# Kernel optimization log

Hardware: AMD Instinct MI355X
Metric: run time of the kernel (lower is better)

## Reference

```python
import jax, jax.numpy as jnp
import numpy as np

D_K = 1024
NHEADS = 16
HEAD_DIM = D_K // NHEADS  # 64
STD = float(np.sqrt(HEAD_DIM))  # matches math.sqrt(d_k // nheads)


def setup_inputs() -> dict:
    key = jax.random.key(0)
    ks = jax.random.split(key, 9)
    B, S = 2, 2048
    scale = 1.0 / np.sqrt(D_K)
    x = jax.random.normal(ks[0], (B, S, D_K), dtype=jnp.float32)
    Wq = jax.random.normal(ks[1], (D_K, D_K), dtype=jnp.float32) * scale
    bq = jnp.zeros((D_K,), dtype=jnp.float32)
    Wk = jax.random.normal(ks[2], (D_K, D_K), dtype=jnp.float32) * scale
    bk = jnp.zeros((D_K,), dtype=jnp.float32)
    Wv = jax.random.normal(ks[3], (D_K, D_K), dtype=jnp.float32) * scale
    bv = jnp.zeros((D_K,), dtype=jnp.float32)
    Wo = jax.random.normal(ks[4], (D_K, D_K), dtype=jnp.float32) * scale
    bo = jnp.zeros((D_K,), dtype=jnp.float32)
    return {"x": x, "Wq": Wq, "bq": bq, "Wk": Wk, "bk": bk,
            "Wv": Wv, "bv": bv, "Wo": Wo, "bo": bo}


def _heads(x, W, b):
    # Linear then split heads: (B,S,D) -> (B,H,S,hd)
    B, S, _ = x.shape
    out = x @ W.T + b
    return out.reshape(B, S, NHEADS, HEAD_DIM).transpose(0, 2, 1, 3)


def reference(x, Wq, bq, Wk, bk, Wv, bv, Wo, bo):
    B, S, _ = x.shape
    q = _heads(x, Wq, bq)  # (B,H,S,hd)
    k = _heads(x, Wk, bk)
    v = _heads(x, Wv, bv)
    scores = jnp.einsum('bhqd,bhkd->bhqk', q, k) / STD  # (B,H,S,S)
    causal = jnp.tril(jnp.ones((S, S), dtype=bool))  # mask_factory default
    scores = jnp.where(causal[None, None, :, :], scores, -jnp.inf)
    attn = jax.nn.softmax(scores, axis=-1)
    ctx = jnp.einsum('bhqk,bhkd->bhqd', attn, v)  # (B,H,S,hd)
    ctx = ctx.transpose(0, 2, 1, 3).reshape(B, S, D_K)
    return ctx @ Wo.T + bo
```

## Files before the change

### kernel.cpp

```cpp
#include <hip/hip_runtime.h>
#include <stdint.h>

typedef unsigned short u16;
typedef __bf16 bf16x8 __attribute__((ext_vector_type(8)));
typedef __bf16 bf16x4v __attribute__((ext_vector_type(4)));
typedef float f32x4 __attribute__((ext_vector_type(4)));

typedef __attribute__((address_space(3))) uint32_t lds_u32;
typedef __attribute__((address_space(1))) uint32_t glb_u32;

__device__ __forceinline__ f32x4 mfma16(bf16x8 a, bf16x8 b, f32x4 c) {
    return __builtin_amdgcn_mfma_f32_16x16x32_bf16(a, b, c, 0, 0, 0);
}

__device__ __forceinline__ ushort4 pk4(float a, float b, float c, float d) {
    bf16x4v v;
    v[0] = (__bf16)a; v[1] = (__bf16)b; v[2] = (__bf16)c; v[3] = (__bf16)d;
    union { bf16x4v v; ushort4 u; } cv; cv.v = v; return cv.u;
}

__device__ __forceinline__ float fexp2(float x) {
    return __builtin_amdgcn_exp2f(x);
}

__device__ __forceinline__ void async16(const u16* g, u16* l) {
    __builtin_amdgcn_global_load_lds((glb_u32*)(uintptr_t)(const void*)g,
                                     (lds_u32*)l, 16, 0, 0);
}

__global__ __launch_bounds__(256) void cast_all(
    const float* __restrict__ x,
    const float* __restrict__ w0, const float* __restrict__ w1,
    const float* __restrict__ w2, const float* __restrict__ w3,
    u16* __restrict__ xo, u16* __restrict__ o0, u16* __restrict__ o1,
    u16* __restrict__ o2, u16* __restrict__ o3)
{
    const int s = blockIdx.y;
    const int i = (blockIdx.x * 256 + threadIdx.x) * 4;
    if (s == 0) {
#pragma unroll
        for (int c = 0; c < 4; ++c) {
            const int j = i + c * (1 << 20);
            float4 v = *(const float4*)(x + j);
            *(ushort4*)(xo + j) = pk4(v.x, v.y, v.z, v.w);
        }
    } else {
        const float* in = s == 1 ? w0 : (s == 2 ? w1 : (s == 3 ? w2 : w3));
        u16* out       = s == 1 ? o0 : (s == 2 ? o1 : (s == 3 ? o2 : o3));
        float4 v = *(const float4*)(in + i);
        *(ushort4*)(out + i) = pk4(v.x, v.y, v.z, v.w);
    }
}

__global__ __launch_bounds__(256) void gemm_qkv(
    const u16* __restrict__ A,
    const u16* __restrict__ W0, const u16* __restrict__ W1, const u16* __restrict__ W2,
    const float* __restrict__ B0, const float* __restrict__ B1, const float* __restrict__ B2,
    u16* __restrict__ O0, u16* __restrict__ O1,
    u16* __restrict__ VT,
    int M, int N, int K)
{
    const int x = blockIdx.x & 7;
    const int L = blockIdx.x >> 3;
    const int tm = (8 * (x >> 1) + (L & 7)) << 7;
    const int tnsel = 12 * (x & 1) + (L >> 3);
    const int sel = tnsel >> 3;
    const int tn  = (tnsel & 7) << 7;

    const u16* W      = sel == 0 ? W0 : (sel == 1 ? W1 : W2);
    const float* bias = sel == 0 ? B0 : (sel == 1 ? B1 : B2);
    u16* O            = sel == 0 ? O0 : O1;

    __shared__ __attribute__((aligned(16))) u16 As[2][128 * 64];
    __shared__ __attribute__((aligned(16))) u16 Bs[2][128 * 64];
    u16 (*Tb)[136] = (u16 (*)[136])As;

    const int tid  = threadIdx.x;
    const int lane = tid & 63;
    const int w    = tid >> 6;
    const int l15  = lane & 15;
    const int quad = lane >> 4;

    const int wm = (w >> 1) << 6;
    const int wn = (w & 1) << 6;

    f32x4 acc[4][4];
#pragma unroll
    for (int i = 0; i < 4; ++i)
#pragma unroll
        for (int j = 0; j < 4; ++j) acc[i][j] = f32x4{0.f, 0.f, 0.f, 0.f};

    const int lr  = lane >> 3;
    const int lcc = lane & 7;
    const int scc = lcc ^ lr;
    const u16* Ag = A + (size_t)(tm + 32 * w + lr) * K + scc * 8;
    const u16* Wg = W + (size_t)(tn + 32 * w + lr) * K + scc * 8;
    u16* Al = &As[0][(32 * w + lr) * 64 + lcc * 8];
    u16* Bl = &Bs[0][(32 * w + lr) * 64 + lcc * 8];

#define QKV_STAGE(bi, k0)                                                      \
    do {                                                                       \
        _Pragma("unroll")                                                      \
        for (int m = 0; m < 4; ++m) {                                          \
            async16(Ag + (k0) + (size_t)m * 8 * K, Al + (bi) * 8192 + m * 512);\
            async16(Wg + (k0) + (size_t)m * 8 * K, Bl + (bi) * 8192 + m * 512);\
        }                                                                      \
    } while (0)

    const int nt = K >> 6;
    QKV_STAGE(0, 0);
    for (int t = 0; t < nt; ++t) {
        const int cur = t & 1;
        asm volatile("s_waitcnt vmcnt(0)" ::: "memory");
        __syncthreads();
        if (t + 1 < nt) QKV_STAGE(cur ^ 1, (t + 1) * 64);
        const u16* Ab = As[cur];
        const u16* Bb = Bs[cur];
#pragma unroll
        for (int kk = 0; kk < 2; ++kk) {
            bf16x8 a[4], b[4];
#pragma unroll
            for (int i = 0; i < 4; ++i) {
                const int r  = wm + 16 * i + l15;
                const int sl = (kk * 4 + quad) ^ (r & 7);
                a[i] = *(const bf16x8*)&Ab[r * 64 + sl * 8];
            }
#pragma unroll
            for (int j = 0; j < 4; ++j) {
                const int r  = wn + 16 * j + l15;
                const int sl = (kk * 4 + quad) ^ (r & 7);
                b[j] = *(const bf16x8*)&Bb[r * 64 + sl * 8];
            }
#pragma unroll
            for (int i = 0; i < 4; ++i)
#pragma unroll
                for (int j = 0; j < 4; ++j)
                    acc[i][j] = mfma16(a[i], b[j], acc[i][j]);
        }
    }
#undef QKV_STAGE

    if (sel == 2) {
        const int bb = tm >> 11;
        const int s0 = tm & 2047;
        const size_t vtb = ((size_t)bb << 10) + tn;
        for (int c32 = 0; c32 < 128; c32 += 32) {
            __syncthreads();
            if ((c32 >> 6) == (wn >> 6)) {
                const int j0 = (c32 >> 4) & 2;
#pragma unroll
                for (int jj = 0; jj < 2; ++jj) {
                    const int j  = j0 + jj;
                    const int cc = jj * 16 + l15;
                    const float bj = bias[tn + wn + 16 * j + l15];
#pragma unroll
                    for (int i = 0; i < 4; ++i) {
                        const int rr = wm + 16 * i + quad * 4;
                        *(ushort4*)&Tb[cc][rr] =
                            pk4(acc[i][j][0] + bj, acc[i][j][1] + bj,
                                acc[i][j][2] + bj, acc[i][j][3] + bj);
                    }
                }
            }
            __syncthreads();
            {
                const int c  = tid >> 3;
                const int ss = (tid & 7) * 16;
                uint4 v0 = *(const uint4*)&Tb[c][ss];
                uint4 v1 = *(const uint4*)&Tb[c][ss + 8];
                u16* dst = &VT[(vtb + c32 + c) * 2048 + s0 + ss];
                *(uint4*)dst       = v0;
                *(uint4*)(dst + 8) = v1;
            }
        }
    } else {
#pragma unroll
        for (int j = 0; j < 4; ++j) {
            const int col = tn + wn + 16 * j + l15;
            const float bj = bias[col];
#pragma unroll
            for (int i = 0; i < 4; ++i) {
                const int row = tm + wm + 16 * i + quad * 4;
#pragma unroll
                for (int r = 0; r < 4; ++r) {
                    union { float f; unsigned u; } v; v.f = acc[i][j][r] + bj;
                    unsigned rn = v.u + 0x7FFFu + ((v.u >> 16) & 1u);
                    O[(size_t)(row + r) * N + col] = (u16)(rn >> 16);
                }
            }
        }
    }
}

__global__ __launch_bounds__(256) void gemm_out64(
    const u16* __restrict__ A, const u16* __restrict__ W,
    const float* __restrict__ bias, float* __restrict__ O,
    int M, int N, int K)
{
    __shared__ __attribute__((aligned(16))) u16 As[2][128 * 64];
    __shared__ __attribute__((aligned(16))) u16 Bs[2][64 * 64];

    const int x = blockIdx.x & 7;
    const int L = blockIdx.x >> 3;
    const int tm = (8 * (x >> 1) + (L & 7)) << 7;
    const int tn = (8 * (x & 1) + (L >> 3)) << 6;

    const int tid  = threadIdx.x;
    const int lane = tid & 63;
    const int w    = tid >> 6;
    const int l15  = lane & 15;
    const int quad = lane >> 4;

    const int wm = (w >> 1) << 6;
    const int wn = (w & 1) << 5;

    f32x4 acc[4][2];
#pragma unroll
    for (int i = 0; i < 4; ++i)
#pragma unroll
        for (int j = 0; j < 2; ++j) acc[i][j] = f32x4{0.f, 0.f, 0.f, 0.f};

    const int lr  = lane >> 3;
    const int lcc = lane & 7;
    const int scc = lcc ^ lr;
    const u16* Ag = A + (size_t)(tm + 32 * w + lr) * K + scc * 8;
    const u16* Wg = W + (size_t)(tn + 16 * w + lr) * K + scc * 8;
    u16* Al = &As[0][(32 * w + lr) * 64 + lcc * 8];
    u16* Bl = &Bs[0][(16 * w + lr) * 64 + lcc * 8];

#define OUT_STAGE(bi, k0)                                                      \
    do {                                                                       \
        _Pragma("unroll")                                                      \
        for (int m = 0; m < 4; ++m)                                            \
            async16(Ag + (k0) + (size_t)m * 8 * K, Al + (bi) * 8192 + m * 512);\
        _Pragma("unroll")                                                      \
        for (int m = 0; m < 2; ++m)                                            \
            async16(Wg + (k0) + (size_t)m * 8 * K, Bl + (bi) * 4096 + m * 512);\
    } while (0)

    const int nt = K >> 6;
    OUT_STAGE(0, 0);
    for (int t = 0; t < nt; ++t) {
        const int cur = t & 1;
        asm volatile("s_waitcnt vmcnt(0)" ::: "memory");
        __syncthreads();
        if (t + 1 < nt) OUT_STAGE(cur ^ 1, (t + 1) * 64);
        const u16* Ab = As[cur];
        const u16* Bb = Bs[cur];
#pragma unroll
        for (int kk = 0; kk < 2; ++kk) {
            bf16x8 a[4], b[2];
#pragma unroll
            for (int i = 0; i < 4; ++i) {
                const int r  = wm + 16 * i + l15;
                const int sl = (kk * 4 + quad) ^ (r & 7);
                a[i] = *(const bf16x8*)&Ab[r * 64 + sl * 8];
            }
#pragma unroll
            for (int j = 0; j < 2; ++j) {
                const int r  = wn + 16 * j + l15;
                const int sl = (kk * 4 + quad) ^ (r & 7);
                b[j] = *(const bf16x8*)&Bb[r * 64 + sl * 8];
            }
#pragma unroll
            for (int i = 0; i < 4; ++i)
#pragma unroll
                for (int j = 0; j < 2; ++j)
                    acc[i][j] = mfma16(a[i], b[j], acc[i][j]);
        }
    }
#undef OUT_STAGE

#pragma unroll
    for (int j = 0; j < 2; ++j) {
        const int col = tn + wn + 16 * j + l15;
        const float bj = bias[col];
#pragma unroll
        for (int i = 0; i < 4; ++i) {
            const int row = tm + wm + 16 * i + quad * 4;
#pragma unroll
            for (int r = 0; r < 4; ++r)
                O[(size_t)(row + r) * N + col] = acc[i][j][r] + bj;
        }
    }
}

__device__ __forceinline__ bf16x8 rdt(const u16* base, int t, int l15, int cc) {
    const int r = t * 16 + l15;
    const int c = (cc & 3) ^ ((r >> 1) & 3);
    return *(const bf16x8*)(base + (cc >> 2) * 2048 + r * 32 + c * 8);
}

#define QK_EXP(Z, PROW, QG, MASKED, RSV, KB)                                   \
    do {                                                                       \
        _Pragma("unroll")                                                      \
        for (int t = 0; t < 4; ++t) {                                          \
            float e0 = fexp2(fmaf((Z)[t][0], SC, -16.0f));                     \
            float e1 = fexp2(fmaf((Z)[t][1], SC, -16.0f));                     \
            float e2 = fexp2(fmaf((Z)[t][2], SC, -16.0f));                     \
            float e3 = fexp2(fmaf((Z)[t][3], SC, -16.0f));                     \
            if (MASKED) {                                                      \
                const int kb = (KB) + t * 16 + quad * 4;                       \
                if (kb + 0 > (QG)) e0 = 0.f;                                   \
                if (kb + 1 > (QG)) e1 = 0.f;                                   \
                if (kb + 2 > (QG)) e2 = 0.f;                                   \
                if (kb + 3 > (QG)) e3 = 0.f;                                   \
            }                                                                  \
            (RSV)[0] += e0; (RSV)[1] += e1;                                    \
            (RSV)[2] += e2; (RSV)[3] += e3;                                    \
            *(ushort4*)((PROW) + (((2 * t + whi) ^ sl7) << 3) + woff) =        \
                pk4(e0, e1, e2, e3);                                           \
        }                                                                      \
    } while (0)

__global__ __launch_bounds__(256) void attn9(
    const u16* __restrict__ Q, const u16* __restrict__ Kb,
    const u16* __restrict__ VT, u16* __restrict__ ctx)
{
    __shared__ __attribute__((aligned(16))) u16 Kt[2][4096];
    __shared__ __attribute__((aligned(16))) u16 Vt[3][4096];
    __shared__ __attribute__((aligned(16))) u16 Pt[4][32][64];

    const int tid  = threadIdx.x;
    const int lane = tid & 63;
    const int wid  = tid >> 6;
    const int l15  = lane & 15;
    const int quad = lane >> 4;
    const int sl7  = l15 & 7;
    const int whi  = quad >> 1;
    const int woff = (quad & 1) * 4;

    const int hb = blockIdx.x & 31;
    const int h  = hb & 15, b = hb >> 4;
    const int ti = blockIdx.x >> 5;
    const int g  = (ti < 8) ? ti : 23 - ti;

    const int sL = 4 * g + wid, sH = 127 - sL;
    const int KL = g, KH = 31 - g;

    const size_t rowbase = (size_t)b * 2048;
    const int cbase = h * 64;
    const u16* kbase = Kb + rowbase * 1024 + cbase;
    const u16* vbase = VT + ((size_t)b * 1024 + cbase) * 2048;

    const int qgL = sL * 16 + l15, qgH = sH * 16 + l15;
    const u16* qpL = Q + (rowbase + qgL) * 1024 + cbase + quad * 8;
    const u16* qpH = Q + (rowbase + qgH) * 1024 + cbase + quad * 8;
    const bf16x8 qL0 = *(const bf16x8*)qpL, qL1 = *(const bf16x8*)(qpL + 32);
    const bf16x8 qH0 = *(const bf16x8*)qpH, qH1 = *(const bf16x8*)(qpH + 32);

    const int sr  = tid >> 2;
    const int sc0 = (((tid & 3) ^ ((sr >> 1) & 3)) << 3);
    const u16* kg = kbase + (size_t)sr * 1024 + sc0;
    const u16* vg = vbase + (size_t)sr * 2048 + sc0;

    f32x4 oL[4], oH[4];
#pragma unroll
    for (int i = 0; i < 4; ++i) { oL[i] = f32x4{0,0,0,0}; oH[i] = f32x4{0,0,0,0}; }
    f32x4 rsLv = {0,0,0,0}, rsHv = {0,0,0,0};
    const float SC = 0.18033688011112042f;

    u16 (*ptw)[64] = Pt[wid];
    u16* const prH = &ptw[16 + l15][0];
    u16* const prL = &ptw[l15][0];

    async16(kg,      &Kt[0][tid * 8]);
    async16(kg + 32, &Kt[0][2048 + tid * 8]);
    async16(vg,      &Vt[0][tid * 8]);
    async16(vg + 32, &Vt[0][2048 + tid * 8]);

    bf16x8 pbH0 = {}, pbH1 = {}, pbL0 = {}, pbL1 = {};
    bool doLp = false;
    int c3 = 0;

    for (int kt = 0; kt <= KH; ++kt) {
        const int curK = kt & 1, nxtK = curK ^ 1;
        const int n3 = (c3 == 2) ? 0 : c3 + 1;
        const int p3 = 3 - c3 - n3;
        asm volatile("s_waitcnt vmcnt(0)" ::: "memory");
        __syncthreads();
        if (kt < KH) {
            const u16* kgn = kg + (size_t)(kt + 1) * 65536;
            const u16* vgn = vg + (kt + 1) * 64;
            async16(kgn,      &Kt[nxtK][tid * 8]);
            async16(kgn + 32, &Kt[nxtK][2048 + tid * 8]);
            async16(vgn,      &Vt[n3][tid * 8]);
            async16(vgn + 32, &Vt[n3][2048 + tid * 8]);
        }
        const u16* KT = Kt[curK];
        const bool doL = (kt <= KL);
        const bool mH = (kt == KH), mL = (kt == KL);

        f32x4 zH[4], zL[4];
        __builtin_amdgcn_s_setprio(1);
        if (doL) {
#pragma unroll
            for (int t = 0; t < 4; ++t) {
                const bf16x8 kA = rdt(KT, t, l15, quad);
                const bf16x8 kB = rdt(KT, t, l15, quad + 4);
                f32x4 zh = {0,0,0,0};
                zh = mfma16(kA, qH0, zh);
                zh = mfma16(kB, qH1, zh);
                zH[t] = zh;
                f32x4 zl = {0,0,0,0};
                zl = mfma16(kA, qL0, zl);
                zl = mfma16(kB, qL1, zl);
                zL[t] = zl;
            }
        } else {
#pragma unroll
            for (int t = 0; t < 4; ++t) {
                const bf16x8 kA = rdt(KT, t, l15, quad);
                const bf16x8 kB = rdt(KT, t, l15, quad + 4);
                f32x4 zh = {0,0,0,0};
                zh = mfma16(kA, qH0, zh);
                zh = mfma16(kB, qH1, zh);
                zH[t] = zh;
            }
        }
        if (kt > 0) {
            const u16* VP = Vt[p3];
            if (doLp) {
#pragma unroll
                for (int t = 0; t < 4; ++t) {
                    const bf16x8 vA = rdt(VP, t, l15, quad);
                    const bf16x8 vB = rdt(VP, t, l15, quad + 4);
                    oH[t] = mfma16(vA, pbH0, oH[t]);
                    oH[t] = mfma16(vB, pbH1, oH[t]);
                    oL[t] = mfma16(vA, pbL0, oL[t]);
                    oL[t] = mfma16(vB, pbL1, oL[t]);
                }
            } else {
#pragma unroll
                for (int t = 0; t < 4; ++t) {
                    const bf16x8 vA = rdt(VP, t, l15, quad);
                    const bf16x8 vB = rdt(VP, t, l15, quad + 4);
                    oH[t] = mfma16(vA, pbH0, oH[t]);
                    oH[t] = mfma16(vB, pbH1, oH[t]);
                }
            }
        }
        __builtin_amdgcn_s_setprio(0);

        const int ktb = kt * 64;
        if (mH) QK_EXP(zH, prH, qgH, 1, rsHv, ktb);
        else    QK_EXP(zH, prH, qgH, 0, rsHv, ktb);
        if (doL) {
            if (mL) QK_EXP(zL, prL, qgL, 1, rsLv, ktb);
            else    QK_EXP(zL, prL, qgL, 0, rsLv, ktb);
        }

        pbH0 = *(const bf16x8*)(prH + ((quad ^ sl7) << 3));
        pbH1 = *(const bf16x8*)(prH + (((quad | 4) ^ sl7) << 3));
        if (doL) {
            pbL0 = *(const bf16x8*)(prL + ((quad ^ sl7) << 3));
            pbL1 = *(const bf16x8*)(prL + (((quad | 4) ^ sl7) << 3));
        }
        doLp = doL;
        c3 = n3;
    }

    {
        const int epi3 = (c3 == 0) ? 2 : c3 - 1;
        const u16* VP = Vt[epi3];
        __builtin_amdgcn_s_setprio(1);
#pragma unroll
        for (int t = 0; t < 4; ++t) {
            const bf16x8 vA = rdt(VP, t, l15, quad);
            const bf16x8 vB = rdt(VP, t, l15, quad + 4);
            oH[t] = mfma16(vA, pbH0, oH[t]);
            oH[t] = mfma16(vB, pbH1, oH[t]);
        }
        __builtin_amdgcn_s_setprio(0);
    }

    float rsH = (rsHv[0] + rsHv[1]) + (rsHv[2] + rsHv[3]);
    float rsL = (rsLv[0] + rsLv[1]) + (rsLv[2] + rsLv[3]);
    rsH += __shfl_xor(rsH, 16); rsH += __shfl_xor(rsH, 32);
    rsL += __shfl_xor(rsL, 16); rsL += __shfl_xor(rsL, 32);
    const float iH = 1.0f / rsH, iL = 1.0f / rsL;
#pragma unroll
    for (int t = 0; t < 4; ++t) {
        *(ushort4*)&ctx[(rowbase + qgL) * 1024 + cbase + t * 16 + quad * 4] =
            pk4(oL[t][0] * iL, oL[t][1] * iL, oL[t][2] * iL, oL[t][3] * iL);
        *(ushort4*)&ctx[(rowbase + qgH) * 1024 + cbase + t * 16 + quad * 4] =
            pk4(oH[t][0] * iH, oH[t][1] * iH, oH[t][2] * iH, oH[t][3] * iH);
    }
}

extern "C" void kernel_launch(void* const* d_in, const int* in_sizes, int n_in,
                              void* d_out, int out_size, void* d_ws, size_t ws_size,
                              hipStream_t stream) {
    const float* x  = (const float*)d_in[0];
    const float* Wq = (const float*)d_in[1];
    const float* bq = (const float*)d_in[2];
    const float* Wk = (const float*)d_in[3];
    const float* bk = (const float*)d_in[4];
    const float* Wv = (const float*)d_in[5];
    const float* bv = (const float*)d_in[6];
    const float* Wo = (const float*)d_in[7];
    const float* bo = (const float*)d_in[8];
    float* out = (float*)d_out;

    const int N = 1024, K = 1024;
    const int M = in_sizes[0] / K;
    const size_t MN = (size_t)M * N;
    const size_t WN = (size_t)N * K;

    u16* xb  = (u16*)d_ws;
    u16* wqb = xb  + MN;
    u16* wkb = wqb + WN;
    u16* wvb = wkb + WN;
    u16* wob = wvb + WN;
    u16* q   = wob + WN;
    u16* kb  = q   + MN;
    u16* vt  = kb  + MN;
    u16* ctx = q;

    cast_all<<<dim3(1024, 5), 256, 0, stream>>>(
        x, Wq, Wk, Wv, Wo, xb, wqb, wkb, wvb, wob);

    gemm_qkv<<<dim3(768), 256, 0, stream>>>(
        xb, wqb, wkb, wvb, bq, bk, bv, q, kb, vt, M, N, K);

    attn9<<<dim3(512), 256, 0, stream>>>(q, kb, vt, ctx);

    gemm_out64<<<dim3(512), 256, 0, stream>>>(
        ctx, wob, bo, out, M, N, K);
}
```

Measured before the change: 186.5 us.

## Process two key tiles per barrier with double-buffered 128-key stages

The attention loop now loads two 64-key K/V tiles per stage into double-buffered shared memory and handles them inside one barrier interval. This halves the number of vmcnt waits and __syncthreads. The software pipeline changes: the PV product for tile k0 is interleaved with the QK of tile k1, replacing the old cross-iteration deferral that used a triple-buffered V. Shared memory rises from 5 to 8 K/V slots, which could reduce occupancy. The P buffer is reused within an iteration, so LDS write/read ordering now rests on wave-local sequencing.

```diff
diff --git a/kernel.cpp b/kernel.cpp
--- a/kernel.cpp
+++ b/kernel.cpp
@@ -313,12 +313,65 @@
         }                                                                      \
     } while (0)
 
-__global__ __launch_bounds__(256) void attn9(
+#define QK_TILE(ZH, ZL, KTp, DOL)                                              \
+    do {                                                                       \
+        __builtin_amdgcn_s_setprio(1);                                         \
+        if (DOL) {                                                             \
+            _Pragma("unroll")                                                  \
+            for (int t = 0; t < 4; ++t) {                                      \
+                const bf16x8 kA = rdt(KTp, t, l15, quad);                      \
+                const bf16x8 kB = rdt(KTp, t, l15, quad + 4);                  \
+                f32x4 zh = {0,0,0,0};                                          \
+                zh = mfma16(kA, qH0, zh); zh = mfma16(kB, qH1, zh);            \
+                (ZH)[t] = zh;                                                  \
+                f32x4 zl = {0,0,0,0};                                          \
+                zl = mfma16(kA, qL0, zl); zl = mfma16(kB, qL1, zl);            \
+                (ZL)[t] = zl;                                                  \
+            }                                                                  \
+        } else {                                                               \
+            _Pragma("unroll")                                                  \
+            for (int t = 0; t < 4; ++t) {                                      \
+                const bf16x8 kA = rdt(KTp, t, l15, quad);                      \
+                const bf16x8 kB = rdt(KTp, t, l15, quad + 4);                  \
+                f32x4 zh = {0,0,0,0};                                          \
+                zh = mfma16(kA, qH0, zh); zh = mfma16(kB, qH1, zh);            \
+                (ZH)[t] = zh;                                                  \
+            }                                                                  \
+        }                                                                      \
+        __builtin_amdgcn_s_setprio(0);                                         \
+    } while (0)
+
+#define PV_TILE(VLp, PH0, PH1, PL0, PL1, DOL)                                  \
+    do {                                                                       \
+        __builtin_amdgcn_s_setprio(1);                                         \
+        if (DOL) {                                                             \
+            _Pragma("unroll")                                                  \
+            for (int t = 0; t < 4; ++t) {                                      \
+                const bf16x8 vA = rdt(VLp, t, l15, quad);                      \
+                const bf16x8 vB = rdt(VLp, t, l15, quad + 4);                  \
+                oH[t] = mfma16(vA, PH0, oH[t]);                                \
+                oH[t] = mfma16(vB, PH1, oH[t]);                                \
+                oL[t] = mfma16(vA, PL0, oL[t]);                                \
+                oL[t] = mfma16(vB, PL1, oL[t]);                                \
+            }                                                                  \
+        } else {                                                               \
+            _Pragma("unroll")                                                  \
+            for (int t = 0; t < 4; ++t) {                                      \
+                const bf16x8 vA = rdt(VLp, t, l15, quad);                      \
+                const bf16x8 vB = rdt(VLp, t, l15, quad + 4);                  \
+                oH[t] = mfma16(vA, PH0, oH[t]);                                \
+                oH[t] = mfma16(vB, PH1, oH[t]);                                \
+            }                                                                  \
+        }                                                                      \
+        __builtin_amdgcn_s_setprio(0);                                         \
+    } while (0)
+
+__global__ __launch_bounds__(256) void attn10(
     const u16* __restrict__ Q, const u16* __restrict__ Kb,
     const u16* __restrict__ VT, u16* __restrict__ ctx)
 {
-    __shared__ __attribute__((aligned(16))) u16 Kt[2][4096];
-    __shared__ __attribute__((aligned(16))) u16 Vt[3][4096];
+    __shared__ __attribute__((aligned(16))) u16 Kt[2][2][4096];
+    __shared__ __attribute__((aligned(16))) u16 Vt[2][2][4096];
     __shared__ __attribute__((aligned(16))) u16 Pt[4][32][64];
 
     const int tid  = threadIdx.x;
@@ -337,6 +390,7 @@
 
     const int sL = 4 * g + wid, sH = 127 - sL;
     const int KL = g, KH = 31 - g;
+    const int NT = (KH + 2) >> 1;
 
     const size_t rowbase = (size_t)b * 2048;
     const int cbase = h * 64;
@@ -363,116 +417,81 @@
     u16 (*ptw)[64] = Pt[wid];
     u16* const prH = &ptw[16 + l15][0];
     u16* const prL = &ptw[l15][0];
-
-    async16(kg,      &Kt[0][tid * 8]);
-    async16(kg + 32, &Kt[0][2048 + tid * 8]);
-    async16(vg,      &Vt[0][tid * 8]);
-    async16(vg + 32, &Vt[0][2048 + tid * 8]);
-
-    bf16x8 pbH0 = {}, pbH1 = {}, pbL0 = {}, pbL1 = {};
-    bool doLp = false;
-    int c3 = 0;
-
-    for (int kt = 0; kt <= KH; ++kt) {
-        const int curK = kt & 1, nxtK = curK ^ 1;
-        const int n3 = (c3 == 2) ? 0 : c3 + 1;
-        const int p3 = 3 - c3 - n3;
+    const int pof0 = (quad ^ sl7) << 3;
+    const int pof1 = ((quad | 4) ^ sl7) << 3;
+
+#define STAGE(buf, Tt)                                                         \
+    do {                                                                       \
+        const u16* kq = kg + (size_t)(Tt) * 131072;                            \
+        const u16* vq = vg + (Tt) * 128;                                       \
+        async16(kq,          &Kt[buf][0][tid * 8]);                            \
+        async16(kq + 32,     &Kt[buf][0][2048 + tid * 8]);                     \
+        async16(kq + 65536,  &Kt[buf][1][tid * 8]);                            \
+        async16(kq + 65568,  &Kt[buf][1][2048 + tid * 8]);                     \
+        async16(vq,          &Vt[buf][0][tid * 8]);                            \
+        async16(vq + 32,     &Vt[buf][0][2048 + tid * 8]);                     \
+        async16(vq + 64,     &Vt[buf][1][tid * 8]);                            \
+        async16(vq + 96,     &Vt[buf][1][2048 + tid * 8]);                     \
+    } while (0)
+
+    STAGE(0, 0);
+
+    for (int T = 0; T < NT; ++T) {
+        const int cur = T & 1;
         asm volatile("s_waitcnt vmcnt(0)" ::: "memory");
         __syncthreads();
-        if (kt < KH) {
-            const u16* kgn = kg + (size_t)(kt + 1) * 65536;
-            const u16* vgn = vg + (kt + 1) * 64;
-            async16(kgn,      &Kt[nxtK][tid * 8]);
-            async16(kgn + 32, &Kt[nxtK][2048 + tid * 8]);
-            async16(vgn,      &Vt[n3][tid * 8]);
-            async16(vgn + 32, &Vt[n3][2048 + tid * 8]);
-        }
-        const u16* KT = Kt[curK];
-        const bool doL = (kt <= KL);
-        const bool mH = (kt == KH), mL = (kt == KL);
-
-        f32x4 zH[4], zL[4];
-        __builtin_amdgcn_s_setprio(1);
-        if (doL) {
-#pragma unroll
-            for (int t = 0; t < 4; ++t) {
-                const bf16x8 kA = rdt(KT, t, l15, quad);
-                const bf16x8 kB = rdt(KT, t, l15, quad + 4);
-                f32x4 zh = {0,0,0,0};
-                zh = mfma16(kA, qH0, zh);
-                zh = mfma16(kB, qH1, zh);
-                zH[t] = zh;
-                f32x4 zl = {0,0,0,0};
-                zl = mfma16(kA, qL0, zl);
-                zl = mfma16(kB, qL1, zl);
-                zL[t] = zl;
-            }
-        } else {
-#pragma unroll
-            for (int t = 0; t < 4; ++t) {
-                const bf16x8 kA = rdt(KT, t, l15, quad);
-                const bf16x8 kB = rdt(KT, t, l15, quad + 4);
-                f32x4 zh = {0,0,0,0};
-                zh = mfma16(kA, qH0, zh);
-                zh = mfma16(kB, qH1, zh);
-                zH[t] = zh;
-            }
-        }
-        if (kt > 0) {
-            const u16* VP = Vt[p3];
-            if (doLp) {
-#pragma unroll
-                for (int t = 0; t < 4; ++t) {
-                    const bf16x8 vA = rdt(VP, t, l15, quad);
-                    const bf16x8 vB = rdt(VP, t, l15, quad + 4);
-                    oH[t] = mfma16(vA, pbH0, oH[t]);
-                    oH[t] = mfma16(vB, pbH1, oH[t]);
-                    oL[t] = mfma16(vA, pbL0, oL[t]);
-                    oL[t] = mfma16(vB, pbL1, oL[t]);
-                }
-            } else {
-#pragma unroll
-                for (int t = 0; t < 4; ++t) {
-                    const bf16x8 vA = rdt(VP, t, l15, quad);
-                    const bf16x8 vB = rdt(VP, t, l15, quad + 4);
-                    oH[t] = mfma16(vA, pbH0, oH[t]);
-                    oH[t] = mfma16(vB, pbH1, oH[t]);
-                }
-            }
-        }
-        __builtin_amdgcn_s_setprio(0);
-
-        const int ktb = kt * 64;
-        if (mH) QK_EXP(zH, prH, qgH, 1, rsHv, ktb);
-        else    QK_EXP(zH, prH, qgH, 0, rsHv, ktb);
-        if (doL) {
-            if (mL) QK_EXP(zL, prL, qgL, 1, rsLv, ktb);
-            else    QK_EXP(zL, prL, qgL, 0, rsLv, ktb);
-        }
-
-        pbH0 = *(const bf16x8*)(prH + ((quad ^ sl7) << 3));
-        pbH1 = *(const bf16x8*)(prH + (((quad | 4) ^ sl7) << 3));
-        if (doL) {
-            pbL0 = *(const bf16x8*)(prL + ((quad ^ sl7) << 3));
-            pbL1 = *(const bf16x8*)(prL + (((quad | 4) ^ sl7) << 3));
-        }
-        doLp = doL;
-        c3 = n3;
-    }
-
-    {
-        const int epi3 = (c3 == 0) ? 2 : c3 - 1;
-        const u16* VP = Vt[epi3];
-        __builtin_amdgcn_s_setprio(1);
-#pragma unroll
-        for (int t = 0; t < 4; ++t) {
-            const bf16x8 vA = rdt(VP, t, l15, quad);
-            const bf16x8 vB = rdt(VP, t, l15, quad + 4);
-            oH[t] = mfma16(vA, pbH0, oH[t]);
-            oH[t] = mfma16(vB, pbH1, oH[t]);
-        }
-        __builtin_amdgcn_s_setprio(0);
-    }
+        if (T + 1 < NT) STAGE(cur ^ 1, T + 1);
+
+        const int k0 = 2 * T, k1 = k0 + 1;
+        const bool has1 = (k1 <= KH);
+        const bool doL0 = (k0 <= KL), doL1 = (k1 <= KL);
+        const bool mH0 = (k0 == KH), mL0 = (k0 == KL);
+        const bool mH1 = (k1 == KH), mL1 = (k1 == KL);
+
+        const u16* KT0 = Kt[cur][0];
+        const u16* KT1 = Kt[cur][1];
+        const u16* VL0 = Vt[cur][0];
+        const u16* VL1 = Vt[cur][1];
+
+        f32x4 zH0[4], zL0[4];
+        QK_TILE(zH0, zL0, KT0, doL0);
+        if (mH0) QK_EXP(zH0, prH, qgH, 1, rsHv, k0 * 64);
+        else     QK_EXP(zH0, prH, qgH, 0, rsHv, k0 * 64);
+        if (doL0) {
+            if (mL0) QK_EXP(zL0, prL, qgL, 1, rsLv, k0 * 64);
+            else     QK_EXP(zL0, prL, qgL, 0, rsLv, k0 * 64);
+        }
+        bf16x8 p0H0 = *(const bf16x8*)(prH + pof0);
+        bf16x8 p0H1 = *(const bf16x8*)(prH + pof1);
+        bf16x8 p0L0 = {}, p0L1 = {};
+        if (doL0) {
+            p0L0 = *(const bf16x8*)(prL + pof0);
+            p0L1 = *(const bf16x8*)(prL + pof1);
+        }
+
+        f32x4 zH1[4], zL1[4];
+        if (has1) QK_TILE(zH1, zL1, KT1, doL1);
+
+        PV_TILE(VL0, p0H0, p0H1, p0L0, p0L1, doL0);
+
+        if (has1) {
+            if (mH1) QK_EXP(zH1, prH, qgH, 1, rsHv, k1 * 64);
+            else     QK_EXP(zH1, prH, qgH, 0, rsHv, k1 * 64);
+            if (doL1) {
+                if (mL1) QK_EXP(zL1, prL, qgL, 1, rsLv, k1 * 64);
+                else     QK_EXP(zL1, prL, qgL, 0, rsLv, k1 * 64);
+            }
+            bf16x8 p1H0 = *(const bf16x8*)(prH + pof0);
+            bf16x8 p1H1 = *(const bf16x8*)(prH + pof1);
+            bf16x8 p1L0 = {}, p1L1 = {};
+            if (doL1) {
+                p1L0 = *(const bf16x8*)(prL + pof0);
+                p1L1 = *(const bf16x8*)(prL + pof1);
+            }
+            PV_TILE(VL1, p1H0, p1H1, p1L0, p1L1, doL1);
+        }
+    }
+#undef STAGE
 
     float rsH = (rsHv[0] + rsHv[1]) + (rsHv[2] + rsHv[3]);
     float rsL = (rsLv[0] + rsLv[1]) + (rsLv[2] + rsLv[3]);
@@ -523,7 +542,7 @@
     gemm_qkv<<<dim3(768), 256, 0, stream>>>(
         xb, wqb, wkb, wvb, bq, bk, bv, q, kb, vt, M, N, K);
 
-    attn9<<<dim3(512), 256, 0, stream>>>(q, kb, vt, ctx);
+    attn10<<<dim3(512), 256, 0, stream>>>(q, kb, vt, ctx);
 
     gemm_out64<<<dim3(512), 256, 0, stream>>>(
         ctx, wob, bo, out, M, N, K);
```

New measurement: 184.7 us. No clear change (-1.0%).

## Split paired low/high query tiles into separate blocks, doubling attention grid

Applied to the files above, without the earlier changes.

Each attention block now handles one 64-row query tile instead of a paired low/high tile, so the grid grows from 512 to 1024 blocks. The software-pipelined PV step that lagged one iteration behind QK is replaced by an in-iteration QK→exp→PV sequence with double-buffered K/V, which shrinks LDS and register use and permits a min-blocks-per-CU launch bound of 4. Blocks are ordered so that tiles with heavy and light causal work interleave. The aim is higher occupancy and more parallelism, at the cost of losing the QK/PV overlap inside a wave and of uneven work per block.

```diff
diff --git a/kernel.cpp b/kernel.cpp
--- a/kernel.cpp
+++ b/kernel.cpp
@@ -313,13 +313,13 @@
         }                                                                      \
     } while (0)
 
-__global__ __launch_bounds__(256) void attn9(
+__global__ __launch_bounds__(256, 4) void attn11(
     const u16* __restrict__ Q, const u16* __restrict__ Kb,
     const u16* __restrict__ VT, u16* __restrict__ ctx)
 {
     __shared__ __attribute__((aligned(16))) u16 Kt[2][4096];
-    __shared__ __attribute__((aligned(16))) u16 Vt[3][4096];
-    __shared__ __attribute__((aligned(16))) u16 Pt[4][32][64];
+    __shared__ __attribute__((aligned(16))) u16 Vt[2][4096];
+    __shared__ __attribute__((aligned(16))) u16 Pt[4][16][64];
 
     const int tid  = threadIdx.x;
     const int lane = tid & 63;
@@ -333,158 +333,98 @@
     const int hb = blockIdx.x & 31;
     const int h  = hb & 15, b = hb >> 4;
     const int ti = blockIdx.x >> 5;
-    const int g  = (ti < 8) ? ti : 23 - ti;
-
-    const int sL = 4 * g + wid, sH = 127 - sL;
-    const int KL = g, KH = 31 - g;
+    const int tq = ti >> 3, to = ti & 7;
+    const int g4 = (tq == 0) ? to
+                 : (tq == 1) ? (15 - to)
+                 : (tq == 2) ? (16 + to)
+                 :             (31 - to);
+    const int s  = 4 * g4 + wid;
+    const int NT = g4 + 1;
 
     const size_t rowbase = (size_t)b * 2048;
     const int cbase = h * 64;
     const u16* kbase = Kb + rowbase * 1024 + cbase;
     const u16* vbase = VT + ((size_t)b * 1024 + cbase) * 2048;
 
-    const int qgL = sL * 16 + l15, qgH = sH * 16 + l15;
-    const u16* qpL = Q + (rowbase + qgL) * 1024 + cbase + quad * 8;
-    const u16* qpH = Q + (rowbase + qgH) * 1024 + cbase + quad * 8;
-    const bf16x8 qL0 = *(const bf16x8*)qpL, qL1 = *(const bf16x8*)(qpL + 32);
-    const bf16x8 qH0 = *(const bf16x8*)qpH, qH1 = *(const bf16x8*)(qpH + 32);
+    const int qg = s * 16 + l15;
+    const u16* qp = Q + (rowbase + qg) * 1024 + cbase + quad * 8;
+    const bf16x8 q0 = *(const bf16x8*)qp, q1 = *(const bf16x8*)(qp + 32);
 
     const int sr  = tid >> 2;
     const int sc0 = (((tid & 3) ^ ((sr >> 1) & 3)) << 3);
     const u16* kg = kbase + (size_t)sr * 1024 + sc0;
     const u16* vg = vbase + (size_t)sr * 2048 + sc0;
 
-    f32x4 oL[4], oH[4];
-#pragma unroll
-    for (int i = 0; i < 4; ++i) { oL[i] = f32x4{0,0,0,0}; oH[i] = f32x4{0,0,0,0}; }
-    f32x4 rsLv = {0,0,0,0}, rsHv = {0,0,0,0};
+    f32x4 o[4];
+#pragma unroll
+    for (int i = 0; i < 4; ++i) o[i] = f32x4{0, 0, 0, 0};
+    f32x4 rsv = {0, 0, 0, 0};
     const float SC = 0.18033688011112042f;
 
     u16 (*ptw)[64] = Pt[wid];
-    u16* const prH = &ptw[16 + l15][0];
-    u16* const prL = &ptw[l15][0];
-
-    async16(kg,      &Kt[0][tid * 8]);
-    async16(kg + 32, &Kt[0][2048 + tid * 8]);
-    async16(vg,      &Vt[0][tid * 8]);
-    async16(vg + 32, &Vt[0][2048 + tid * 8]);
-
-    bf16x8 pbH0 = {}, pbH1 = {}, pbL0 = {}, pbL1 = {};
-    bool doLp = false;
-    int c3 = 0;
-
-    for (int kt = 0; kt <= KH; ++kt) {
-        const int curK = kt & 1, nxtK = curK ^ 1;
-        const int n3 = (c3 == 2) ? 0 : c3 + 1;
-        const int p3 = 3 - c3 - n3;
+    u16* const pr = &ptw[l15][0];
+    const int pof0 = (quad ^ sl7) << 3;
+    const int pof1 = ((quad | 4) ^ sl7) << 3;
+
+#define STAGE(buf, Tt)                                                         \
+    do {                                                                       \
+        const u16* kq = kg + (size_t)(Tt) * 65536;                             \
+        const u16* vq = vg + (Tt) * 64;                                        \
+        async16(kq,      &Kt[buf][tid * 8]);                                   \
+        async16(kq + 32, &Kt[buf][2048 + tid * 8]);                            \
+        async16(vq,      &Vt[buf][tid * 8]);                                   \
+        async16(vq + 32, &Vt[buf][2048 + tid * 8]);                            \
+    } while (0)
+
+    STAGE(0, 0);
+
+    for (int T = 0; T < NT; ++T) {
+        const int cur = T & 1;
         asm volatile("s_waitcnt vmcnt(0)" ::: "memory");
         __syncthreads();
-        if (kt < KH) {
-            const u16* kgn = kg + (size_t)(kt + 1) * 65536;
-            const u16* vgn = vg + (kt + 1) * 64;
-            async16(kgn,      &Kt[nxtK][tid * 8]);
-            async16(kgn + 32, &Kt[nxtK][2048 + tid * 8]);
-            async16(vgn,      &Vt[n3][tid * 8]);
-            async16(vgn + 32, &Vt[n3][2048 + tid * 8]);
-        }
-        const u16* KT = Kt[curK];
-        const bool doL = (kt <= KL);
-        const bool mH = (kt == KH), mL = (kt == KL);
-
-        f32x4 zH[4], zL[4];
+        if (T + 1 < NT) STAGE(cur ^ 1, T + 1);
+
+        const u16* KT = Kt[cur];
+        const u16* VL = Vt[cur];
+
+        f32x4 z[4];
         __builtin_amdgcn_s_setprio(1);
-        if (doL) {
-#pragma unroll
-            for (int t = 0; t < 4; ++t) {
-                const bf16x8 kA = rdt(KT, t, l15, quad);
-                const bf16x8 kB = rdt(KT, t, l15, quad + 4);
-                f32x4 zh = {0,0,0,0};
-                zh = mfma16(kA, qH0, zh);
-                zh = mfma16(kB, qH1, zh);
-                zH[t] = zh;
-                f32x4 zl = {0,0,0,0};
-                zl = mfma16(kA, qL0, zl);
-                zl = mfma16(kB, qL1, zl);
-                zL[t] = zl;
-            }
-        } else {
-#pragma unroll
-            for (int t = 0; t < 4; ++t) {
-                const bf16x8 kA = rdt(KT, t, l15, quad);
-                const bf16x8 kB = rdt(KT, t, l15, quad + 4);
-                f32x4 zh = {0,0,0,0};
-                zh = mfma16(kA, qH0, zh);
-                zh = mfma16(kB, qH1, zh);
-                zH[t] = zh;
-            }
-        }
-        if (kt > 0) {
-            const u16* VP = Vt[p3];
-            if (doLp) {
-#pragma unroll
-                for (int t = 0; t < 4; ++t) {
-                    const bf16x8 vA = rdt(VP, t, l15, quad);
-                    const bf16x8 vB = rdt(VP, t, l15, quad + 4);
-                    oH[t] = mfma16(vA, pbH0, oH[t]);
-                    oH[t] = mfma16(vB, pbH1, oH[t]);
-                    oL[t] = mfma16(vA, pbL0, oL[t]);
-                    oL[t] = mfma16(vB, pbL1, oL[t]);
-                }
-            } else {
-#pragma unroll
-                for (int t = 0; t < 4; ++t) {
-                    const bf16x8 vA = rdt(VP, t, l15, quad);
-                    const bf16x8 vB = rdt(VP, t, l15, quad + 4);
-                    oH[t] = mfma16(vA, pbH0, oH[t]);
-                    oH[t] = mfma16(vB, pbH1, oH[t]);
-                }
-            }
+#pragma unroll
+        for (int t = 0; t < 4; ++t) {
+            const bf16x8 kA = rdt(KT, t, l15, quad);
+            const bf16x8 kB = rdt(KT, t, l15, quad + 4);
+            f32x4 zz = {0, 0, 0, 0};
+            zz = mfma16(kA, q0, zz);
+            zz = mfma16(kB, q1, zz);
+            z[t] = zz;
         }
         __builtin_amdgcn_s_setprio(0);
 
-        const int ktb = kt * 64;
-        if (mH) QK_EXP(zH, prH, qgH, 1, rsHv, ktb);
-        else    QK_EXP(zH, prH, qgH, 0, rsHv, ktb);
-        if (doL) {
-            if (mL) QK_EXP(zL, prL, qgL, 1, rsLv, ktb);
-            else    QK_EXP(zL, prL, qgL, 0, rsLv, ktb);
-        }
-
-        pbH0 = *(const bf16x8*)(prH + ((quad ^ sl7) << 3));
-        pbH1 = *(const bf16x8*)(prH + (((quad | 4) ^ sl7) << 3));
-        if (doL) {
-            pbL0 = *(const bf16x8*)(prL + ((quad ^ sl7) << 3));
-            pbL1 = *(const bf16x8*)(prL + (((quad | 4) ^ sl7) << 3));
-        }
-        doLp = doL;
-        c3 = n3;
-    }
-
-    {
-        const int epi3 = (c3 == 0) ? 2 : c3 - 1;
-        const u16* VP = Vt[epi3];
+        if (T == NT - 1) QK_EXP(z, pr, qg, 1, rsv, T * 64);
+        else             QK_EXP(z, pr, qg, 0, rsv, T * 64);
+
+        const bf16x8 pb0 = *(const bf16x8*)(pr + pof0);
+        const bf16x8 pb1 = *(const bf16x8*)(pr + pof1);
+
         __builtin_amdgcn_s_setprio(1);
 #pragma unroll
         for (int t = 0; t < 4; ++t) {
-            const bf16x8 vA = rdt(VP, t, l15, quad);
-            const bf16x8 vB = rdt(VP, t, l15, quad + 4);
-            oH[t] = mfma16(vA, pbH0, oH[t]);
-            oH[t] = mfma16(vB, pbH1, oH[t]);
+            const bf16x8 vA = rdt(VL, t, l15, quad);
+            const bf16x8 vB = rdt(VL, t, l15, quad + 4);
+            o[t] = mfma16(vA, pb0, o[t]);
+            o[t] = mfma16(vB, pb1, o[t]);
         }
         __builtin_amdgcn_s_setprio(0);
     }
-
-    float rsH = (rsHv[0] + rsHv[1]) + (rsHv[2] + rsHv[3]);
-    float rsL = (rsLv[0] + rsLv[1]) + (rsLv[2] + rsLv[3]);
-    rsH += __shfl_xor(rsH, 16); rsH += __shfl_xor(rsH, 32);
-    rsL += __shfl_xor(rsL, 16); rsL += __shfl_xor(rsL, 32);
-    const float iH = 1.0f / rsH, iL = 1.0f / rsL;
+#undef STAGE
+
+    float rs = (rsv[0] + rsv[1]) + (rsv[2] + rsv[3]);
+    rs += __shfl_xor(rs, 16); rs += __shfl_xor(rs, 32);
+    const float inv = 1.0f / rs;
 #pragma unroll
     for (int t = 0; t < 4; ++t) {
-        *(ushort4*)&ctx[(rowbase + qgL) * 1024 + cbase + t * 16 + quad * 4] =
-            pk4(oL[t][0] * iL, oL[t][1] * iL, oL[t][2] * iL, oL[t][3] * iL);
-        *(ushort4*)&ctx[(rowbase + qgH) * 1024 + cbase + t * 16 + quad * 4] =
-            pk4(oH[t][0] * iH, oH[t][1] * iH, oH[t][2] * iH, oH[t][3] * iH);
+        *(ushort4*)&ctx[(rowbase + qg) * 1024 + cbase + t * 16 + quad * 4] =
+            pk4(o[t][0] * inv, o[t][1] * inv, o[t][2] * inv, o[t][3] * inv);
     }
 }
 
@@ -523,7 +463,7 @@
     gemm_qkv<<<dim3(768), 256, 0, stream>>>(
         xb, wqb, wkb, wvb, bq, bk, bv, q, kb, vt, M, N, K);
 
-    attn9<<<dim3(512), 256, 0, stream>>>(q, kb, vt, ctx);
+    attn11<<<dim3(1024), 256, 0, stream>>>(q, kb, vt, ctx);
 
     gemm_out64<<<dim3(512), 256, 0, stream>>>(
         ctx, wob, bo, out, M, N, K);
```

New measurement: 178.2 us. -4.5%, faster.
